# Kernel optimization log

Hardware: AMD Instinct MI355X
Metric: run time of the kernel (lower is better)

The kernel has to match this reference:

```python
import jax, jax.numpy as jnp
import numpy as np

N_NODES, N_EDGES, NNZ = 10000, 4000, 30000
IN_CH, HEADS, OUT_CH = 128, 2, 64


def _scale2_pattern(node, edge, num_nodes, num_edges):
    """Sparsity pattern of H @ (H^T H) where H is the node x edge incidence.
    Mirrors torch.sparse.mm + coalesce + (values > 0) mask (pattern only,
    since all values are positive sums of ones)."""
    # unique incidence pattern (coalesce)
    uk = np.unique(node.astype(np.int64) * num_edges + edge.astype(np.int64))
    n_u, e_u = uk // num_edges, uk % num_edges
    # --- stage 1: pattern of H^T H = edge pairs sharing a node ---
    order = np.argsort(n_u, kind="stable")
    ns, es = n_u[order], e_u[order]
    _, starts, cnts = np.unique(ns, return_index=True, return_counts=True)
    cpe = np.repeat(cnts, cnts)          # group size per sorted entry
    gpe = np.repeat(starts, cnts)        # group start per sorted entry
    tot = int(cpe.sum())
    within = np.arange(tot) - np.repeat(np.cumsum(cpe) - cpe, cpe)
    pe = np.repeat(es, cpe)
    pep = es[np.repeat(gpe, cpe) + within]
    pk = np.unique(pe * num_edges + pep)
    pe, pep = pk // num_edges, pk % num_edges
    # --- stage 2: pattern of H @ (H^T H) ---
    po = np.argsort(pe, kind="stable")
    pe_s, pep_s = pe[po], pep[po]
    cnt_e = np.bincount(pe_s, minlength=num_edges)
    ptr = np.concatenate([np.zeros(1, np.int64), np.cumsum(cnt_e)])
    c2 = cnt_e[e_u]
    tot2 = int(c2.sum())
    within2 = np.arange(tot2) - np.repeat(np.cumsum(c2) - c2, c2)
    v2 = np.repeat(n_u, c2)
    ep2 = pep_s[ptr[e_u].repeat(c2) + within2]
    k2 = np.unique(v2 * num_edges + ep2)
    return k2 // num_edges, k2 % num_edges


def setup_inputs() -> dict:
    rng = np.random.default_rng(0)
    node1 = rng.integers(0, N_NODES, NNZ).astype(np.int64)
    edge1 = rng.integers(0, N_EDGES, NNZ).astype(np.int64)
    node2, edge2 = _scale2_pattern(node1, edge1, N_NODES, N_EDGES)

    key = jax.random.key(0)
    k = jax.random.split(key, 4)
    HO = HEADS * OUT_CH
    xav1 = (2.0 / (IN_CH + HO)) ** 0.5
    xavo = (2.0 / (HO + OUT_CH)) ** 0.5
    return {
        "x": jax.random.normal(k[0], (N_NODES, IN_CH), jnp.float32),
        "hyperedge_index1": jnp.asarray(np.stack([node1, edge1]), jnp.int32),
        "hyperedge_index2": jnp.asarray(np.stack([node2, edge2]), jnp.int32),
        "W1": jax.random.normal(k[1], (HO, IN_CH), jnp.float32) * xav1,
        "b1": jnp.zeros((HO,), jnp.float32),
        "W2": jax.random.normal(k[2], (HO, IN_CH), jnp.float32) * xav1,
        "b2": jnp.zeros((HO,), jnp.float32),
        "Wout": jax.random.normal(k[3], (OUT_CH, HO), jnp.float32) * xavo,
        "bout": jnp.zeros((OUT_CH,), jnp.float32),
        "num_edges": N_EDGES,
    }


def _hconv(x, W, b, node_idx, edge_idx, num_edges):
    num_nodes = x.shape[0]
    xt = x @ W.T + b                                  # [N, H*O]
    g = xt[node_idx]                                  # [nnz, H*O] gather
    esum = jax.ops.segment_sum(g, edge_idx, num_segments=num_edges)
    cnt = jax.ops.segment_sum(jnp.ones(edge_idx.shape, xt.dtype), edge_idx,
                              num_segments=num_edges)
    emean = esum / jnp.maximum(cnt, 1.0)[:, None]     # scatter_mean (0 if empty)
    return jax.ops.segment_sum(emean[edge_idx], node_idx,
                               num_segments=num_nodes)  # scatter_add


def reference(x, hyperedge_index1, hyperedge_index2, W1, b1, W2, b2, Wout, bout,
              num_edges):
    o1 = _hconv(x, W1, b1, hyperedge_index1[0], hyperedge_index1[1], num_edges)
    o2 = _hconv(x, W2, b2, hyperedge_index2[0], hyperedge_index2[1], num_edges)
    o = 0.5 * (o1 + o2)                               # mean over 2 scales
    return o @ Wout.T + bout                          # output_proj
```

## Files before the change

kernel.cpp:

```cpp
#include <hip/hip_runtime.h>
#include <hip/hip_bf16.h>

#define N_NODES 10000
#define N_EDGES 4000
#define IN_CH   128
#define CHUNK   16384

#define G_GEMM  625
#define G_NPTR  40

__device__ __forceinline__ float bf2f(unsigned short u) {
    union { unsigned int i; float f; } v;
    v.i = ((unsigned int)u) << 16;
    return v.f;
}
__device__ __forceinline__ unsigned short f2bfu(float f) {
    union { __hip_bfloat16 h; unsigned short u; } v;
    v.h = __float2bfloat16(f);
    return v.u;
}

__device__ __forceinline__ void load8(const void* base, size_t eoff, int isf32,
                                      float o[8]) {
    if (isf32) {
        const float4* q = (const float4*)((const float*)base + eoff);
        float4 a = q[0], b = q[1];
        o[0]=a.x; o[1]=a.y; o[2]=a.z; o[3]=a.w;
        o[4]=b.x; o[5]=b.y; o[6]=b.z; o[7]=b.w;
    } else {
        uint4 v = *(const uint4*)((const unsigned short*)base + eoff);
        const unsigned short* pv = (const unsigned short*)&v;
#pragma unroll
        for (int q = 0; q < 8; q++) o[q] = bf2f(pv[q]);
    }
}

__device__ __forceinline__ float loadS(const void* base, int i, int isf32) {
    return isf32 ? ((const float*)base)[i] : bf2f(((const unsigned short*)base)[i]);
}

__device__ __forceinline__ int probe_isf32(const unsigned int* __restrict__ x) {
    const int lane = threadIdx.x & 63;
    unsigned int w0 = x[lane * 2], w1 = x[lane * 2 + 1];
    int h = 0, z = 0;
    {
        unsigned int lo = w0 & 0xFFFFu;
        if (lo == 0u) z++; else if (((lo >> 7) & 0xFF) >= 0x90u) h++;
        lo = w1 & 0xFFFFu;
        if (lo == 0u) z++; else if (((lo >> 7) & 0xFF) >= 0x90u) h++;
    }
    unsigned long long bh = __ballot(h > 0);
    unsigned long long bz = __ballot(z == 2);
    return (__popcll(bh) > 8 || __popcll(bz) > 50) ? 1 : 0;
}

__device__ __forceinline__ void add4(float acc[4], uint2 u) {
    acc[0] += bf2f((unsigned short)(u.x & 0xFFFFu));
    acc[1] += bf2f((unsigned short)(u.x >> 16));
    acc[2] += bf2f((unsigned short)(u.y & 0xFFFFu));
    acc[3] += bf2f((unsigned short)(u.y >> 16));
}

__device__ __forceinline__ void block_scan1024(const int* __restrict__ cnt,
                                               int nb, int* __restrict__ out,
                                               int* __restrict__ wsum)
{
    const int t = threadIdx.x;
    const int lane = t & 63, wid = t >> 6;
    const int K = (nb + 1023) >> 10;
    const int base = t * K;
    int s = 0;
    for (int q = 0; q < K; q++) { int i = base + q; s += (i < nb) ? cnt[i] : 0; }
    int inc = s;
#pragma unroll
    for (int d = 1; d < 64; d <<= 1) {
        int v = __shfl_up(inc, d);
        if (lane >= d) inc += v;
    }
    if (lane == 63) wsum[wid] = inc;
    __syncthreads();
    if (t < 16) {
        int v = wsum[t];
#pragma unroll
        for (int d = 1; d < 16; d <<= 1) {
            int u = __shfl_up(v, d);
            if (t >= d) v += u;
        }
        wsum[t] = v;
    }
    __syncthreads();
    const int wbase = (wid == 0) ? 0 : wsum[wid - 1];
    int run = wbase + inc - s;
    for (int q = 0; q < K; q++) {
        int i = base + q;
        if (i < nb) { out[i] = run; run += cnt[i]; }
    }
    if (t == 1023) out[nb] = wsum[15];
    __syncthreads();
}

__global__ __launch_bounds__(256) void weff_zero(
    const void* __restrict__ Wout,
    const void* __restrict__ W1, const void* __restrict__ b1,
    const void* __restrict__ W2, const void* __restrict__ b2,
    float* __restrict__ weff1, float* __restrict__ beff1,
    float* __restrict__ weff2, float* __restrict__ beff2,
    int* __restrict__ cntz, int* __restrict__ fillz,
    const unsigned int* __restrict__ xprobe)
{
    const int b = blockIdx.x;
    if (b == 4) {
        for (int t = threadIdx.x; t < 18000; t += 256) cntz[t] = 0;
        for (int t = threadIdx.x; t < 14000; t += 256) fillz[t] = 0;
        return;
    }
    __shared__ float wsh[64][IN_CH];
    const int isf32 = probe_isf32(xprobe);

    if (b == 5) {
        float* bsh = &wsh[0][0];
        const int t = threadIdx.x;
        {
            const int s = t >> 7, h = t & 127;
            bsh[t] = loadS(s ? b2 : b1, h, isf32);
        }
        __syncthreads();
        if (t < 128) {
            const int s = t >> 6, o = t & 63;
            float a = 0.f;
#pragma unroll 4
            for (int r = 0; r < 16; r++) {
                float v[8];
                load8(Wout, (size_t)o * 128 + r * 8, isf32, v);
#pragma unroll
                for (int q = 0; q < 8; q++) a += v[q] * bsh[s * 128 + r * 8 + q];
            }
            (s ? beff2 : beff1)[o] = 0.5f * a;
        }
        return;
    }

    const int s  = b >> 1;
    const int oh = b & 1;
    const void* Ws = s ? W2 : W1;
    float* outW = s ? weff2 : weff1;
    const int o  = oh * 32 + (threadIdx.x >> 3);
    const int i0 = (threadIdx.x & 7) * 16;
    float acc[16];
#pragma unroll
    for (int k = 0; k < 16; k++) acc[k] = 0.f;

    for (int pass = 0; pass < 2; pass++) {
        if (pass) __syncthreads();
        for (int r = 0; r < 4; r++) {
            int idx = r * 2048 + threadIdx.x * 8;
            float v[8];
            load8(Ws, (size_t)pass * 8192 + idx, isf32, v);
            float* d = &wsh[0][0] + idx;
#pragma unroll
            for (int q = 0; q < 8; q++) d[q] = v[q];
        }
        float wrow[64];
#pragma unroll
        for (int r = 0; r < 8; r++) {
            float v[8];
            load8(Wout, (size_t)o * 128 + pass * 64 + r * 8, isf32, v);
#pragma unroll
            for (int q = 0; q < 8; q++) wrow[r * 8 + q] = v[q];
        }
        __syncthreads();
#pragma unroll 4
        for (int h = 0; h < 64; h++) {
            const float wo = wrow[h];
            const float* wr = &wsh[h][i0];
#pragma unroll
            for (int k = 0; k < 16; k++) acc[k] += wo * wr[k];
        }
    }
#pragma unroll
    for (int k = 0; k < 16; k++)
        outW[o * 128 + i0 + k] = 0.5f * acc[k];
}

__global__ __launch_bounds__(256) void prep(
    const void* __restrict__ x,
    const float* __restrict__ weff1, const float* __restrict__ beff1,
    const float* __restrict__ weff2, const float* __restrict__ beff2,
    unsigned short* __restrict__ xtP1b, unsigned short* __restrict__ xtP2b,
    const int* __restrict__ idx1, int nnz1,
    const int* __restrict__ idx2, int nnz2,
    int* __restrict__ nptr,
    int* __restrict__ bh, int* __restrict__ cnt2,
    int* __restrict__ cnt1e, int* __restrict__ cnt1n, int nblk)
{
    __shared__ __align__(16) char smem[40000];
    int b = blockIdx.x;

    if (b < nblk) {
        int* h = (int*)smem;
        for (int t = threadIdx.x; t < N_EDGES; t += 256) h[t] = 0;
        __syncthreads();
        const int lo = b * CHUNK;
        const int hi = min(nnz2, lo + CHUNK);
        for (int i = lo + threadIdx.x; i < hi; i += 256)
            atomicAdd(&h[idx2[nnz2 + i]], 1);
        __syncthreads();
        int* dst = bh + (size_t)b * N_EDGES;
        for (int t = threadIdx.x; t < N_EDGES; t += 256) {
            int v = h[t];
            dst[t] = v;
            if (v) atomicAdd(&cnt2[t], v);
        }
        return;
    }
    b -= nblk;

    if (b < 8) {
        const int isEdge = b < 4;
        const int bid = isEdge ? b : (b - 4);
        const int nb = isEdge ? N_EDGES : N_NODES;
        const int* src = isEdge ? (idx1 + nnz1) : idx1;
        int* dst = isEdge ? cnt1e : cnt1n;
        int* h = (int*)smem;
        for (int t = threadIdx.x; t < nb; t += 256) h[t] = 0;
        __syncthreads();
        for (int i = bid * 256 + threadIdx.x; i < nnz1; i += 4 * 256)
            atomicAdd(&h[src[i]], 1);
        __syncthreads();
        for (int t = threadIdx.x; t < nb; t += 256) {
            int v = h[t];
            if (v) atomicAdd(&dst[t], v);
        }
        return;
    }
    b -= 8;

    if (b < G_GEMM) {
        const int isf32 = probe_isf32((const unsigned int*)x);
        float (*xs)[IN_CH] = (float (*)[IN_CH])smem;
        const int n0 = b * 16;
        {
            float v[8];
            load8(x, (size_t)n0 * IN_CH + (size_t)threadIdx.x * 8, isf32, v);
            float* dst = &xs[0][0] + threadIdx.x * 8;
#pragma unroll
            for (int q = 0; q < 8; q++) dst[q] = v[q];
        }
        __syncthreads();

        const int g   = threadIdx.x >> 7;
        const int sel = (threadIdx.x >> 6) & 1;
        const int j   = threadIdx.x & 63;
        const float* WE = sel ? weff2 : weff1;
        const float* BE = sel ? beff2 : beff1;
        unsigned short* xtP = sel ? xtP2b : xtP1b;

        float acc[8];
#pragma unroll
        for (int m = 0; m < 8; m++) acc[m] = 0.f;

        const float4* Wr = (const float4*)(WE + (size_t)j * 128);
        for (int kk = 0; kk < 16; kk++) {
            float4 a = Wr[kk * 2], c = Wr[kk * 2 + 1];
            float w[8] = {a.x, a.y, a.z, a.w, c.x, c.y, c.z, c.w};
#pragma unroll
            for (int m = 0; m < 8; m++) {
                const float* xr = &xs[g * 8 + m][kk * 8];
                acc[m] += xr[0]*w[0] + xr[1]*w[1] + xr[2]*w[2] + xr[3]*w[3]
                        + xr[4]*w[4] + xr[5]*w[5] + xr[6]*w[6] + xr[7]*w[7];
            }
        }
        const float bias = BE[j];
#pragma unroll
        for (int m = 0; m < 8; m++)
            xtP[(size_t)(n0 + g * 8 + m) * 64 + j] = f2bfu(acc[m] + bias);
        return;
    }
    b -= G_GEMM;

    {
        int n = b * 256 + threadIdx.x;
        if (n > N_NODES) return;
        int lo = 0, hi = nnz2;
        while (lo < hi) { int mid = (lo + hi) >> 1; if (idx2[mid] < n) lo = mid + 1; else hi = mid; }
        nptr[n] = lo;
    }
}

__global__ __launch_bounds__(1024) void sort_fill(
    const int* __restrict__ cnt2, int* __restrict__ ptr2g,
    const int* __restrict__ bh, int nblk,
    const int* __restrict__ idx2, int nnz2,
    unsigned short* __restrict__ nodelist2,
    const int* __restrict__ idx1, int nnz1,
    const int* __restrict__ cnt1e, int* __restrict__ ptr1eg,
    int* __restrict__ fill1e, unsigned short* __restrict__ nodelist1,
    const int* __restrict__ cnt1n, int* __restrict__ ptr1ng,
    int* __restrict__ fill1n, unsigned short* __restrict__ edgelist1)
{
    __shared__ int sscan[14002];
    __shared__ int wsum[16];
    int b = blockIdx.x;
    const int t = threadIdx.x;

    if (b < nblk) {
        block_scan1024(cnt2, N_EDGES, sscan, wsum);
        if (b == 0)
            for (int i = t; i <= N_EDGES; i += 1024) ptr2g[i] = sscan[i];
        int* lh = sscan + 4001;
        for (int e = t; e < N_EDGES; e += 1024) {
            int acc = sscan[e];
            for (int k = 0; k < b; k++) acc += bh[(size_t)k * N_EDGES + e];
            sscan[e] = acc;
            lh[e] = 0;
        }
        __syncthreads();
        const int lo = b * CHUNK;
        const int hi = min(nnz2, lo + CHUNK);
        for (int i = lo + t; i < hi; i += 1024) {
            int n = idx2[i];
            int e = idx2[nnz2 + i];
            int s = atomicAdd(&lh[e], 1);
            nodelist2[sscan[e] + s] = (unsigned short)n;
        }
        return;
    }
    b -= nblk;
    int* p1e = sscan;
    int* p1n = sscan + 4001;
    block_scan1024(cnt1e, N_EDGES, p1e, wsum);
    block_scan1024(cnt1n, N_NODES, p1n, wsum);
    if (b == 0) {
        for (int i = t; i <= N_EDGES; i += 1024) ptr1eg[i] = p1e[i];
        for (int i = t; i <= N_NODES; i += 1024) ptr1ng[i] = p1n[i];
    }
    int i = b * 1024 + t;
    if (i >= nnz1) return;
    int n = idx1[i];
    int e = idx1[nnz1 + i];
    int se = atomicAdd(&fill1e[e], 1);
    nodelist1[p1e[e] + se] = (unsigned short)n;
    int sn = atomicAdd(&fill1n[n], 1);
    edgelist1[p1n[n] + sn] = (unsigned short)e;
}

__global__ __launch_bounds__(256) void edge_gather(
    const unsigned short* __restrict__ nodelist2, const int* __restrict__ ptr2,
    const unsigned int* __restrict__ xtP2u, unsigned int* __restrict__ emean2b,
    const unsigned short* __restrict__ nodelist1, const int* __restrict__ ptr1e,
    const unsigned int* __restrict__ xtP1u, unsigned int* __restrict__ emean1b)
{
    int b = blockIdx.x;
    if (b < 1000) {
        const int lane = threadIdx.x & 63;
        const int sub  = lane >> 4;
        const int ch4  = lane & 15;
        const int e = b * 4 + (threadIdx.x >> 6);
        const int lo = ptr2[e], hi = ptr2[e + 1];
        const uint2* src2 = (const uint2*)xtP2u;
        float acc[4] = {0.f, 0.f, 0.f, 0.f};
        int i = lo;
        for (; i + 32 <= hi; i += 32) {
            int n[8]; uint2 u[8];
#pragma unroll
            for (int q = 0; q < 8; q++) n[q] = nodelist2[i + 4 * q + sub];
#pragma unroll
            for (int q = 0; q < 8; q++) u[q] = src2[(size_t)n[q] * 16 + ch4];
#pragma unroll
            for (int q = 0; q < 8; q++) add4(acc, u[q]);
        }
        for (; i < hi; i += 4) {
            if (i + sub < hi) {
                int n0 = nodelist2[i + sub];
                add4(acc, src2[(size_t)n0 * 16 + ch4]);
            }
        }
#pragma unroll
        for (int q = 0; q < 4; q++) {
            acc[q] += __shfl_xor(acc[q], 16);
            acc[q] += __shfl_xor(acc[q], 32);
        }
        if (sub == 0) {
            const float inv = 1.f / fmaxf((float)(hi - lo), 1.f);
            uint2 o;
            o.x = ((unsigned int)f2bfu(acc[1] * inv) << 16) | f2bfu(acc[0] * inv);
            o.y = ((unsigned int)f2bfu(acc[3] * inv) << 16) | f2bfu(acc[2] * inv);
            ((uint2*)emean2b)[(size_t)e * 16 + ch4] = o;
        }
        return;
    }
    b -= 1000;
    {
        const int lane = threadIdx.x & 31;
        const int e = b * 8 + (threadIdx.x >> 5);
        const int lo = ptr1e[e], hi = ptr1e[e + 1];
        float accx = 0.f, accy = 0.f;
        for (int base = lo; base < hi; base += 32) {
            const int m = min(32, hi - base);
            int vl = (base + lane < hi) ? (int)nodelist1[base + lane] : 0;
            int t = 0;
            for (; t + 7 < m; t += 8) {
                int nn[8]; unsigned int uu[8];
#pragma unroll
                for (int q = 0; q < 8; q++) nn[q] = __shfl(vl, t + q, 32);
#pragma unroll
                for (int q = 0; q < 8; q++) uu[q] = xtP1u[nn[q] * 32 + lane];
#pragma unroll
                for (int q = 0; q < 8; q++) {
                    accx += bf2f((unsigned short)(uu[q] & 0xFFFFu));
                    accy += bf2f((unsigned short)(uu[q] >> 16));
                }
            }
            for (; t < m; t++) {
                int n = __shfl(vl, t, 32);
                unsigned int u = xtP1u[n * 32 + lane];
                accx += bf2f((unsigned short)(u & 0xFFFFu));
                accy += bf2f((unsigned short)(u >> 16));
            }
        }
        const float inv = 1.f / fmaxf((float)(hi - lo), 1.f);
        emean1b[e * 32 + lane] =
            ((unsigned int)f2bfu(accy * inv) << 16) | f2bfu(accx * inv);
    }
}

__global__ __launch_bounds__(256) void node_final(
    const int* __restrict__ vals2, const int* __restrict__ nptr,
    const unsigned int* __restrict__ emean2b,
    const unsigned short* __restrict__ edgelist1, const int* __restrict__ ptr1n,
    const unsigned int* __restrict__ emean1b,
    const void* __restrict__ bout, void* __restrict__ out,
    const unsigned int* __restrict__ xprobe)
{
    const int isf32 = probe_isf32(xprobe);
    const int lane = threadIdx.x & 63;
    const int sub  = lane >> 4;
    const int ch4  = lane & 15;
    const int n = blockIdx.x * 4 + (threadIdx.x >> 6);
    float acc[4] = {0.f, 0.f, 0.f, 0.f};

    {
        const int lo = nptr[n], hi = nptr[n + 1];
        const uint2* src = (const uint2*)emean2b;
        int i = lo;
        for (; i + 32 <= hi; i += 32) {
            int e[8]; uint2 u[8];
#pragma unroll
            for (int q = 0; q < 8; q++) e[q] = vals2[i + 4 * q + sub];
#pragma unroll
            for (int q = 0; q < 8; q++) u[q] = src[(size_t)e[q] * 16 + ch4];
#pragma unroll
            for (int q = 0; q < 8; q++) add4(acc, u[q]);
        }
        for (; i < hi; i += 4) {
            if (i + sub < hi)
                add4(acc, src[(size_t)vals2[i + sub] * 16 + ch4]);
        }
    }
    {
        const int lo = ptr1n[n], hi = ptr1n[n + 1];
        const uint2* src = (const uint2*)emean1b;
        int i = lo;
        for (; i + 32 <= hi; i += 32) {
            int e[8]; uint2 u[8];
#pragma unroll
            for (int q = 0; q < 8; q++) e[q] = edgelist1[i + 4 * q + sub];
#pragma unroll
            for (int q = 0; q < 8; q++) u[q] = src[(size_t)e[q] * 16 + ch4];
#pragma unroll
            for (int q = 0; q < 8; q++) add4(acc, u[q]);
        }
        for (; i < hi; i += 4) {
            if (i + sub < hi)
                add4(acc, src[(size_t)edgelist1[i + sub] * 16 + ch4]);
        }
    }
#pragma unroll
    for (int q = 0; q < 4; q++) {
        acc[q] += __shfl_xor(acc[q], 16);
        acc[q] += __shfl_xor(acc[q], 32);
    }
    if (sub == 0) {
        float r[4];
#pragma unroll
        for (int q = 0; q < 4; q++)
            r[q] = acc[q] + loadS(bout, ch4 * 4 + q, isf32);
        if (isf32) {
            ((float4*)out)[(size_t)n * 16 + ch4] =
                make_float4(r[0], r[1], r[2], r[3]);
        } else {
            uint2 o;
            o.x = ((unsigned int)f2bfu(r[1]) << 16) | f2bfu(r[0]);
            o.y = ((unsigned int)f2bfu(r[3]) << 16) | f2bfu(r[2]);
            ((uint2*)out)[(size_t)n * 16 + ch4] = o;
        }
    }
}

extern "C" void kernel_launch(void* const* d_in, const int* in_sizes, int n_in,
                              void* d_out, int out_size, void* d_ws, size_t ws_size,
                              hipStream_t stream)
{
    const void* x  = d_in[0];
    const int* idx1 = (const int*)d_in[1];
    const int* idx2 = (const int*)d_in[2];
    const void* W1 = d_in[3];
    const void* b1 = d_in[4];
    const void* W2 = d_in[5];
    const void* b2 = d_in[6];
    const void* Wo = d_in[7];
    const void* bo = d_in[8];

    const int nnz1 = in_sizes[1] / 2;
    const int nnz2 = in_sizes[2] / 2;
    const int nblk = (nnz2 + CHUNK - 1) / CHUNK;
    const int F1p = (nnz1 + 1023) / 1024;

    float* ws = (float*)d_ws;
    unsigned short* xtP1b = (unsigned short*)ws;
    unsigned int*   xtP1u = (unsigned int*)xtP1b;
    unsigned short* xtP2b = (unsigned short*)(ws + 320000);
    unsigned int*   xtP2u = (unsigned int*)xtP2b;
    int*   fill1e = (int*)(ws + 1280000);
    int*   fill1n = (int*)(ws + 1284000);
    int* cnt2  = (int*)(ws + 1550000);
    int* cnt1e = (int*)(ws + 1554000);
    int* cnt1n = (int*)(ws + 1558000);
    int* ptr2  = (int*)(ws + 1568000);
    int* ptr1e = (int*)(ws + 1572004);
    int* ptr1n = (int*)(ws + 1576008);
    int* nptr  = (int*)(ws + 1586012);
    float* weff1 = ws + 1596016;
    float* weff2 = ws + 1604208;
    float* beff1 = ws + 1612400;
    float* beff2 = ws + 1612464;
    unsigned int* emean2b = (unsigned int*)(ws + 1612528);
    unsigned int* emean1b = (unsigned int*)(ws + 1740528);
    unsigned short* nodelist2 = (unsigned short*)(ws + 1868528);
    const size_t nl2u = ((size_t)nnz2 + 1) / 2;
    unsigned short* nodelist1 = (unsigned short*)(ws + 1868528 + nl2u);
    const size_t nl1u = ((size_t)nnz1 + 1) / 2;
    unsigned short* edgelist1 = (unsigned short*)(ws + 1868528 + nl2u + nl1u);
    const size_t bh_off = (1868528 + nl2u + 2 * nl1u + 7) & ~(size_t)7;
    int* bh = (int*)(ws + bh_off);

    weff_zero<<<6, 256, 0, stream>>>(Wo, W1, b1, W2, b2,
                                     weff1, beff1, weff2, beff2,
                                     cnt2, fill1e, (const unsigned int*)x);

    prep<<<nblk + 8 + G_GEMM + G_NPTR, 256, 0, stream>>>(
        x, weff1, beff1, weff2, beff2, xtP1b, xtP2b,
        idx1, nnz1, idx2, nnz2,
        nptr, bh, cnt2, cnt1e, cnt1n, nblk);

    sort_fill<<<nblk + F1p, 1024, 0, stream>>>(
        cnt2, ptr2, bh, nblk,
        idx2, nnz2, nodelist2,
        idx1, nnz1,
        cnt1e, ptr1e, fill1e, nodelist1,
        cnt1n, ptr1n, fill1n, edgelist1);

    edge_gather<<<1000 + N_EDGES / 8, 256, 0, stream>>>(
        nodelist2, ptr2, xtP2u, emean2b,
        nodelist1, ptr1e, xtP1u, emean1b);

    node_final<<<N_NODES / 4, 256, 0, stream>>>(
        idx2 + nnz2, nptr, emean2b, edgelist1, ptr1n, emean1b,
        bo, d_out, (const unsigned int*)x);
}
```

Before: 183.7 us.

## Move node projection GEMM from histogram kernel into sort-fill kernel

Moves the x·Weff projection GEMM blocks out of the prep/histogram kernel and into the sort-fill launch, using 1024-thread blocks that each handle 64 nodes, with tail clamping and guarded stores. This shortens the histogram kernel so the GEMM can run alongside the scatter/fill blocks, balancing work across the two launches. In exchange the GEMM now sits behind the 1024-thread, large-shared-memory footprint of sort_fill, which limits occupancy, and larger blocks mean fewer of them.

```diff
diff --git a/kernel.cpp b/kernel.cpp
--- a/kernel.cpp
+++ b/kernel.cpp
@@ -6,8 +6,8 @@
 #define IN_CH   128
 #define CHUNK   16384
 
-#define G_GEMM  625
 #define G_NPTR  40
+#define NG64    157
 
 __device__ __forceinline__ float bf2f(unsigned short u) {
     union { unsigned int i; float f; } v;
@@ -182,11 +182,7 @@
         outW[o * 128 + i0 + k] = 0.5f * acc[k];
 }
 
-__global__ __launch_bounds__(256) void prep(
-    const void* __restrict__ x,
-    const float* __restrict__ weff1, const float* __restrict__ beff1,
-    const float* __restrict__ weff2, const float* __restrict__ beff2,
-    unsigned short* __restrict__ xtP1b, unsigned short* __restrict__ xtP2b,
+__global__ __launch_bounds__(256) void hist(
     const int* __restrict__ idx1, int nnz1,
     const int* __restrict__ idx2, int nnz2,
     int* __restrict__ nptr,
@@ -235,49 +231,6 @@
     }
     b -= 8;
 
-    if (b < G_GEMM) {
-        const int isf32 = probe_isf32((const unsigned int*)x);
-        float (*xs)[IN_CH] = (float (*)[IN_CH])smem;
-        const int n0 = b * 16;
-        {
-            float v[8];
-            load8(x, (size_t)n0 * IN_CH + (size_t)threadIdx.x * 8, isf32, v);
-            float* dst = &xs[0][0] + threadIdx.x * 8;
-#pragma unroll
-            for (int q = 0; q < 8; q++) dst[q] = v[q];
-        }
-        __syncthreads();
-
-        const int g   = threadIdx.x >> 7;
-        const int sel = (threadIdx.x >> 6) & 1;
-        const int j   = threadIdx.x & 63;
-        const float* WE = sel ? weff2 : weff1;
-        const float* BE = sel ? beff2 : beff1;
-        unsigned short* xtP = sel ? xtP2b : xtP1b;
-
-        float acc[8];
-#pragma unroll
-        for (int m = 0; m < 8; m++) acc[m] = 0.f;
-
-        const float4* Wr = (const float4*)(WE + (size_t)j * 128);
-        for (int kk = 0; kk < 16; kk++) {
-            float4 a = Wr[kk * 2], c = Wr[kk * 2 + 1];
-            float w[8] = {a.x, a.y, a.z, a.w, c.x, c.y, c.z, c.w};
-#pragma unroll
-            for (int m = 0; m < 8; m++) {
-                const float* xr = &xs[g * 8 + m][kk * 8];
-                acc[m] += xr[0]*w[0] + xr[1]*w[1] + xr[2]*w[2] + xr[3]*w[3]
-                        + xr[4]*w[4] + xr[5]*w[5] + xr[6]*w[6] + xr[7]*w[7];
-            }
-        }
-        const float bias = BE[j];
-#pragma unroll
-        for (int m = 0; m < 8; m++)
-            xtP[(size_t)(n0 + g * 8 + m) * 64 + j] = f2bfu(acc[m] + bias);
-        return;
-    }
-    b -= G_GEMM;
-
     {
         int n = b * 256 + threadIdx.x;
         if (n > N_NODES) return;
@@ -287,7 +240,7 @@
     }
 }
 
-__global__ __launch_bounds__(1024) void sort_fill(
+__global__ __launch_bounds__(1024) void sf_gemm(
     const int* __restrict__ cnt2, int* __restrict__ ptr2g,
     const int* __restrict__ bh, int nblk,
     const int* __restrict__ idx2, int nnz2,
@@ -296,7 +249,12 @@
     const int* __restrict__ cnt1e, int* __restrict__ ptr1eg,
     int* __restrict__ fill1e, unsigned short* __restrict__ nodelist1,
     const int* __restrict__ cnt1n, int* __restrict__ ptr1ng,
-    int* __restrict__ fill1n, unsigned short* __restrict__ edgelist1)
+    int* __restrict__ fill1n, unsigned short* __restrict__ edgelist1,
+    const void* __restrict__ x,
+    const float* __restrict__ weff1, const float* __restrict__ beff1,
+    const float* __restrict__ weff2, const float* __restrict__ beff2,
+    unsigned short* __restrict__ xtP1b, unsigned short* __restrict__ xtP2b,
+    int F1p)
 {
     __shared__ int sscan[14002];
     __shared__ int wsum[16];
@@ -326,22 +284,74 @@
         return;
     }
     b -= nblk;
-    int* p1e = sscan;
-    int* p1n = sscan + 4001;
-    block_scan1024(cnt1e, N_EDGES, p1e, wsum);
-    block_scan1024(cnt1n, N_NODES, p1n, wsum);
-    if (b == 0) {
-        for (int i = t; i <= N_EDGES; i += 1024) ptr1eg[i] = p1e[i];
-        for (int i = t; i <= N_NODES; i += 1024) ptr1ng[i] = p1n[i];
-    }
-    int i = b * 1024 + t;
-    if (i >= nnz1) return;
-    int n = idx1[i];
-    int e = idx1[nnz1 + i];
-    int se = atomicAdd(&fill1e[e], 1);
-    nodelist1[p1e[e] + se] = (unsigned short)n;
-    int sn = atomicAdd(&fill1n[n], 1);
-    edgelist1[p1n[n] + sn] = (unsigned short)e;
+
+    if (b < F1p) {
+        int* p1e = sscan;
+        int* p1n = sscan + 4001;
+        block_scan1024(cnt1e, N_EDGES, p1e, wsum);
+        block_scan1024(cnt1n, N_NODES, p1n, wsum);
+        if (b == 0) {
+            for (int i = t; i <= N_EDGES; i += 1024) ptr1eg[i] = p1e[i];
+            for (int i = t; i <= N_NODES; i += 1024) ptr1ng[i] = p1n[i];
+        }
+        int i = b * 1024 + t;
+        if (i >= nnz1) return;
+        int n = idx1[i];
+        int e = idx1[nnz1 + i];
+        int se = atomicAdd(&fill1e[e], 1);
+        nodelist1[p1e[e] + se] = (unsigned short)n;
+        int sn = atomicAdd(&fill1n[n], 1);
+        edgelist1[p1n[n] + sn] = (unsigned short)e;
+        return;
+    }
+    b -= F1p;
+
+    {
+        const int isf32 = probe_isf32((const unsigned int*)x);
+        float (*xs)[IN_CH] = (float (*)[IN_CH])sscan;
+        const int n0 = b * 64;
+        {
+            int idx = t * 8;
+            int row = n0 + (idx >> 7);
+            int srcrow = row < N_NODES ? row : (N_NODES - 1);
+            float v[8];
+            load8(x, (size_t)srcrow * IN_CH + (idx & 127), isf32, v);
+            float* dst = &xs[0][0] + idx;
+#pragma unroll
+            for (int q = 0; q < 8; q++) dst[q] = v[q];
+        }
+        __syncthreads();
+
+        const int g8  = t >> 7;
+        const int sel = (t >> 6) & 1;
+        const int j   = t & 63;
+        const float* WE = sel ? weff2 : weff1;
+        const float* BE = sel ? beff2 : beff1;
+        unsigned short* xtP = sel ? xtP2b : xtP1b;
+
+        float acc[8];
+#pragma unroll
+        for (int m = 0; m < 8; m++) acc[m] = 0.f;
+
+        const float4* Wr = (const float4*)(WE + (size_t)j * 128);
+        for (int kk = 0; kk < 16; kk++) {
+            float4 a = Wr[kk * 2], c = Wr[kk * 2 + 1];
+            float w[8] = {a.x, a.y, a.z, a.w, c.x, c.y, c.z, c.w};
+#pragma unroll
+            for (int m = 0; m < 8; m++) {
+                const float* xr = &xs[g8 * 8 + m][kk * 8];
+                acc[m] += xr[0]*w[0] + xr[1]*w[1] + xr[2]*w[2] + xr[3]*w[3]
+                        + xr[4]*w[4] + xr[5]*w[5] + xr[6]*w[6] + xr[7]*w[7];
+            }
+        }
+        const float bias = BE[j];
+#pragma unroll
+        for (int m = 0; m < 8; m++) {
+            int node = n0 + g8 * 8 + m;
+            if (node < N_NODES)
+                xtP[(size_t)node * 64 + j] = f2bfu(acc[m] + bias);
+        }
+    }
 }
 
 __global__ __launch_bounds__(256) void edge_gather(
@@ -548,17 +558,17 @@
                                      weff1, beff1, weff2, beff2,
                                      cnt2, fill1e, (const unsigned int*)x);
 
-    prep<<<nblk + 8 + G_GEMM + G_NPTR, 256, 0, stream>>>(
-        x, weff1, beff1, weff2, beff2, xtP1b, xtP2b,
+    hist<<<nblk + 8 + G_NPTR, 256, 0, stream>>>(
         idx1, nnz1, idx2, nnz2,
         nptr, bh, cnt2, cnt1e, cnt1n, nblk);
 
-    sort_fill<<<nblk + F1p, 1024, 0, stream>>>(
+    sf_gemm<<<nblk + F1p + NG64, 1024, 0, stream>>>(
         cnt2, ptr2, bh, nblk,
         idx2, nnz2, nodelist2,
         idx1, nnz1,
         cnt1e, ptr1e, fill1e, nodelist1,
-        cnt1n, ptr1n, fill1n, edgelist1);
+        cnt1n, ptr1n, fill1n, edgelist1,
+        x, weff1, beff1, weff2, beff2, xtP1b, xtP2b, F1p);
 
     edge_gather<<<1000 + N_EDGES / 8, 256, 0, stream>>>(
         nodelist2, ptr2, xtP2u, emean2b,
```

Measured after the change: 186.8 us. About the same (+1.7%).
